# Performance work log

Hardware: AMD Instinct MI355X
Metric: run time of the kernel (lower is better)

Reference implementation:

```python
import jax, jax.numpy as jnp
import numpy as np

N_CODEBOOKS = 4
N_EMBED = 1024
EMBED_DIM = 64
PATCH = 4
BETA = 0.25
EPS = 1e-5
USAGE_W = 0.01


def setup_inputs() -> dict:
    key = jax.random.key(0)
    k1, k2 = jax.random.split(key)
    z = jax.random.normal(k1, (8, 64, 128, 128), dtype=jnp.float32)
    # one EMA codebook per quantizer, initialized ~ randn like torch buffer
    codebooks = jax.random.normal(k2, (N_CODEBOOKS, N_EMBED, EMBED_DIM), dtype=jnp.float32)
    return {"z": z, "codebooks": codebooks}


def _usage_loss(indices, n_embed):
    # negative-entropy penalty on code usage (no gradient path: counts are ints)
    counts = jnp.bincount(indices.reshape(-1), length=n_embed).astype(jnp.float32)
    probs = (counts + EPS) / (counts.sum() + EPS * n_embed)
    entropy = -jnp.sum(probs * jnp.log(probs + EPS))
    return jnp.log(jnp.float32(n_embed)) - entropy


def _ema_quantize(residual, embedding):
    # residual: [N, C, ph, pw], embedding: [n_e, C]; eval mode (no EMA buffer update)
    N, C, ph, pw = residual.shape
    z_flat = residual.transpose(0, 2, 3, 1).reshape(-1, C)  # [M, C]
    d = (jnp.sum(z_flat ** 2, axis=1, keepdims=True)
         + jnp.sum(embedding ** 2, axis=1)
         - 2.0 * z_flat @ embedding.T)  # [M, n_e]
    idx = jnp.argmin(d, axis=1)  # [M]
    z_q = embedding[idx].reshape(N, ph, pw, C).transpose(0, 3, 1, 2)  # [N, C, ph, pw]
    loss = BETA * jnp.mean((jax.lax.stop_gradient(z_q) - residual) ** 2)
    z_q_st = residual + jax.lax.stop_gradient(z_q - residual)  # straight-through
    return z_q_st, loss, idx.reshape(N, ph, pw)


def reference(z, codebooks):
    B, C, H, W = z.shape
    h, w = H // PATCH, W // PATCH
    # b c (h ph) (w pw) -> (b h w) c ph pw
    zp = (z.reshape(B, C, h, PATCH, w, PATCH)
            .transpose(0, 2, 4, 1, 3, 5)
            .reshape(B * h * w, C, PATCH, PATCH))
    zq_acc = jnp.zeros_like(zp)
    residual = zp
    losses, all_idx = [], []
    for i in range(N_CODEBOOKS):
        zq_i, loss_i, idx_i = _ema_quantize(residual, codebooks[i])
        loss_i = loss_i + USAGE_W * _usage_loss(idx_i, N_EMBED)
        zq_acc = zq_acc + zq_i
        residual = residual - zq_i
        losses.append(loss_i)
        all_idx.append(idx_i.reshape(idx_i.shape[0], -1))  # [N, ph*pw]
    loss = jnp.stack(losses).sum()
    # (b h w) c ph pw -> b c (h ph) (w pw)
    z_q = (zq_acc.reshape(B, h, w, C, PATCH, PATCH)
                 .transpose(0, 3, 1, 4, 2, 5)
                 .reshape(B, C, H, W))
    # [N, patch_area, n_codebooks] -> [b, h, w, patch_area, n_codebooks]
    min_idx = jnp.stack(all_idx, axis=-1).reshape(B, h, w, PATCH * PATCH, N_CODEBOOKS)
    return z_q, loss, min_idx
```

## Files before the change

kernel.cpp:

```cpp
#include <hip/hip_runtime.h>
#include <math.h>

typedef __attribute__((ext_vector_type(8))) short short8;
typedef __attribute__((ext_vector_type(4))) float f32x4;

#define NCB 4
#define NE 1024
#define DIM 64
#define HW 16384
#define NPIX 131072
#define NWAVES 4096
#define MSE_DENOM 8388608.0f
#define EPSF 1e-5f
#define CHUNK_BYTES 24576
#define CHUNK_SHORTS 12288
#define NCHUNK 16

__device__ __forceinline__ unsigned short f2bf(float x) {
    unsigned u = __float_as_uint(x);
    u += 0x7fffu + ((u >> 16) & 1u);
    return (unsigned short)(u >> 16);
}
__device__ __forceinline__ float bf2f(unsigned short h) {
    return __uint_as_float(((unsigned)h) << 16);
}

__global__ __launch_bounds__(64) void rvq_norms(const float* __restrict__ cb,
                                                float* __restrict__ nrmh) {
    int code = blockIdx.x * 64 + threadIdx.x;
    const float4* row = reinterpret_cast<const float4*>(cb + (size_t)code * DIM);
    float s0 = 0.f, s1 = 0.f, s2 = 0.f, s3 = 0.f;
#pragma unroll
    for (int k = 0; k < 16; ++k) {
        float4 v = row[k];
        s0 = fmaf(v.x, v.x, s0); s1 = fmaf(v.y, v.y, s1);
        s2 = fmaf(v.z, v.z, s2); s3 = fmaf(v.w, v.w, s3);
    }
    nrmh[code] = -0.5f * ((s0 + s1) + (s2 + s3));
}

__global__ __launch_bounds__(256) void rvq_presplit(const float* __restrict__ cb,
                                                    unsigned short* __restrict__ gB) {
    int blk = blockIdx.x;
    int tid = threadIdx.x;
    int code = tid >> 2, dg = tid & 3;
    int c0 = (blk & 15) << 6;
    int i  = blk >> 4;
    const float4* s4 = reinterpret_cast<const float4*>(
        cb + ((size_t)i * NE + c0 + code) * DIM + dg * 16);
    float v[16];
    {
        float4 q;
        q = s4[0]; v[0]=q.x; v[1]=q.y; v[2]=q.z; v[3]=q.w;
        q = s4[1]; v[4]=q.x; v[5]=q.y; v[6]=q.z; v[7]=q.w;
        q = s4[2]; v[8]=q.x; v[9]=q.y; v[10]=q.z; v[11]=q.w;
        q = s4[3]; v[12]=q.x; v[13]=q.y; v[14]=q.z; v[15]=q.w;
    }
    char* outc = reinterpret_cast<char*>(gB + (size_t)blk * CHUNK_SHORTS);
    int linbase = code * 128 + dg * 32;
    int sw = (code & 7) << 4;
#pragma unroll
    for (int h = 0; h < 2; ++h) {
        short8 p1, p2, p3;
#pragma unroll
        for (int e = 0; e < 8; ++e) {
            float t = v[h * 8 + e];
            unsigned short u1 = f2bf(t); t -= bf2f(u1);
            unsigned short u2 = f2bf(t); t -= bf2f(u2);
            unsigned short u3 = f2bf(t);
            p1[e] = (short)u1; p2[e] = (short)u2; p3[e] = (short)u3;
        }
        int a = (linbase + h * 16) ^ sw;
        *reinterpret_cast<short8*>(outc + a)         = p1;
        *reinterpret_cast<short8*>(outc + 8192 + a)  = p2;
        *reinterpret_cast<short8*>(outc + 16384 + a) = p3;
    }
}

__device__ __forceinline__ void gload16(const void* gsrc, void* ldst) {
    __builtin_amdgcn_global_load_lds(
        (const __attribute__((address_space(1))) unsigned int*)gsrc,
        (__attribute__((address_space(3))) unsigned int*)ldst, 16, 0, 0);
}

__global__ __launch_bounds__(256, 2) void rvq_main(
    const float* __restrict__ z, const unsigned short* __restrict__ gB,
    const float* __restrict__ nrmh, const float* __restrict__ cb,
    float* __restrict__ out_zq, float* __restrict__ out_idx,
    unsigned* __restrict__ hist, float* __restrict__ msePartial)
{
    __shared__ uint4 sB[2][CHUNK_BYTES / 16];
    __shared__ int   sBest[4][32];

    const int tid  = threadIdx.x;
    const int lane = tid & 63;
    const int wid  = tid >> 6;
    const int col  = lane & 15;
    const int g    = lane >> 4;
    const int blockPix = blockIdx.x * 128;
    char* sBase = reinterpret_cast<char*>(sB);
    const int sw = (col & 7) << 4;

#pragma unroll
    for (int k = 0; k < 6; ++k)
        gload16(reinterpret_cast<const char*>(gB) + k * 4096 + tid * 16,
                sBase + k * 4096 + tid * 16);

    size_t zb[2];
#pragma unroll
    for (int m = 0; m < 2; ++m) {
        int pf = blockPix + wid * 32 + m * 16 + col;
        zb[m] = (size_t)(pf >> 14) * 1048576 + (size_t)(pf & 16383);
    }

    float r[2][2][8];
#pragma unroll
    for (int m = 0; m < 2; ++m)
#pragma unroll
        for (int kh = 0; kh < 2; ++kh)
#pragma unroll
            for (int e = 0; e < 8; ++e)
                r[m][kh][e] = z[zb[m] + (size_t)(kh * 32 + g * 8 + e) * HW];

    for (int i = 0; i < NCB; ++i) {
        const char* gBi = reinterpret_cast<const char*>(gB) + (size_t)i * NCHUNK * CHUNK_BYTES;
        const float* nrm_i = nrmh + i * NE;

        short8 A[3][2][2];
#pragma unroll
        for (int m = 0; m < 2; ++m)
#pragma unroll
            for (int kh = 0; kh < 2; ++kh)
#pragma unroll
                for (int e = 0; e < 8; ++e) {
                    float t = r[m][kh][e];
                    unsigned short u1 = f2bf(t); t -= bf2f(u1);
                    unsigned short u2 = f2bf(t); t -= bf2f(u2);
                    unsigned short u3 = f2bf(t);
                    A[0][m][kh][e] = (short)u1;
                    A[1][m][kh][e] = (short)u2;
                    A[2][m][kh][e] = (short)u3;
                }

        float maxv[2][4]; int maxi[2][4];
#pragma unroll
        for (int m = 0; m < 2; ++m)
#pragma unroll
            for (int rr = 0; rr < 4; ++rr) { maxv[m][rr] = -3.4e38f; maxi[m][rr] = 0; }

        for (int c = 0; c < NCHUNK; ++c) {
            __syncthreads();
            if (c < NCHUNK - 1) {
                const char* gc = gBi + (size_t)(c + 1) * CHUNK_BYTES;
                char* sbn = sBase + ((c + 1) & 1) * CHUNK_BYTES;
#pragma unroll
                for (int k = 0; k < 6; ++k)
                    gload16(gc + k * 4096 + tid * 16, sbn + k * 4096 + tid * 16);
            }
            const char* sbc = sBase + (c & 1) * CHUNK_BYTES;

#pragma unroll
            for (int sub = 0; sub < 4; ++sub) {
                const int code = (sub << 4) + col;
                float nh = nrm_i[(c << 6) + code];
                f32x4 acc[2];
#pragma unroll
                for (int rr = 0; rr < 4; ++rr) { acc[0][rr] = nh; acc[1][rr] = nh; }

                __builtin_amdgcn_s_setprio(1);
#pragma unroll
                for (int sb = 0; sb < 3; ++sb) {
                    short8 B0 = *reinterpret_cast<const short8*>(
                        sbc + sb * 8192 + ((((code << 7) + (g << 4))) ^ sw));
                    short8 B1 = *reinterpret_cast<const short8*>(
                        sbc + sb * 8192 + ((((code << 7) + 64 + (g << 4))) ^ sw));
#pragma unroll
                    for (int sa = 0; sa < 3 - sb; ++sa) {
                        acc[0] = __builtin_amdgcn_mfma_f32_16x16x32_bf16(A[sa][0][0], B0, acc[0], 0, 0, 0);
                        acc[1] = __builtin_amdgcn_mfma_f32_16x16x32_bf16(A[sa][1][0], B0, acc[1], 0, 0, 0);
                        acc[0] = __builtin_amdgcn_mfma_f32_16x16x32_bf16(A[sa][0][1], B1, acc[0], 0, 0, 0);
                        acc[1] = __builtin_amdgcn_mfma_f32_16x16x32_bf16(A[sa][1][1], B1, acc[1], 0, 0, 0);
                    }
                }
                __builtin_amdgcn_s_setprio(0);

#pragma unroll
                for (int m = 0; m < 2; ++m)
#pragma unroll
                    for (int rr = 0; rr < 4; ++rr) {
                        float s = acc[m][rr];
                        if (s > maxv[m][rr]) { maxv[m][rr] = s; maxi[m][rr] = (c << 6) + code; }
                    }
            }
        }

        if (i < NCB - 1) {
            const char* gn = reinterpret_cast<const char*>(gB)
                           + (size_t)(i + 1) * NCHUNK * CHUNK_BYTES;
#pragma unroll
            for (int k = 0; k < 6; ++k)
                gload16(gn + k * 4096 + tid * 16, sBase + k * 4096 + tid * 16);
        }

#pragma unroll
        for (int m = 0; m < 2; ++m)
#pragma unroll
            for (int rr = 0; rr < 4; ++rr) {
                float v = maxv[m][rr]; int ix = maxi[m][rr];
#pragma unroll
                for (int off = 1; off < 16; off <<= 1) {
                    float ov = __shfl_xor(v, off, 64);
                    int   oi = __shfl_xor(ix, off, 64);
                    if (ov > v || (ov == v && oi < ix)) { v = ov; ix = oi; }
                }
                maxi[m][rr] = ix;
            }
        if (col == 0) {
#pragma unroll
            for (int m = 0; m < 2; ++m)
#pragma unroll
                for (int rr = 0; rr < 4; ++rr)
                    sBest[wid][m * 16 + g * 4 + rr] = maxi[m][rr];
        }

        const float* cbi = cb + (size_t)i * NE * DIM;
        if (lane < 16) {
#pragma unroll
            for (int m = 0; m < 2; ++m) {
                int pfr = blockPix + wid * 32 + m * 16 + lane;
                int bb = pfr >> 14, yy = (pfr >> 7) & 127, xx = pfr & 127;
                int bi = sBest[wid][m * 16 + lane];
                size_t off = (size_t)bb * 65536 + (size_t)(yy >> 2) * 2048
                           + (size_t)(xx >> 2) * 64
                           + (size_t)(((yy & 3) << 2) + (xx & 3)) * 4 + (size_t)i;
                out_idx[off] = (float)bi;
                atomicAdd(&hist[i * NE + bi], 1u);
            }
        }

#pragma unroll
        for (int m = 0; m < 2; ++m) {
            const int best = sBest[wid][m * 16 + col];
            const float* er = cbi + (size_t)best * DIM;
#pragma unroll
            for (int kh = 0; kh < 2; ++kh) {
                const float4* e4 = reinterpret_cast<const float4*>(er + kh * 32 + g * 8);
                float4 q0 = e4[0], q1 = e4[1];
                r[m][kh][0] -= q0.x; r[m][kh][1] -= q0.y;
                r[m][kh][2] -= q0.z; r[m][kh][3] -= q0.w;
                r[m][kh][4] -= q1.x; r[m][kh][5] -= q1.y;
                r[m][kh][6] -= q1.z; r[m][kh][7] -= q1.w;
            }
        }

        float s = 0.f;
#pragma unroll
        for (int m = 0; m < 2; ++m)
#pragma unroll
            for (int kh = 0; kh < 2; ++kh)
#pragma unroll
                for (int e = 0; e < 8; ++e) s = fmaf(r[m][kh][e], r[m][kh][e], s);
#pragma unroll
        for (int d_ = 32; d_ > 0; d_ >>= 1) s += __shfl_down(s, d_, 64);
        if (lane == 0) msePartial[i * NWAVES + blockIdx.x * 4 + wid] = s;
    }

#pragma unroll
    for (int m = 0; m < 2; ++m)
#pragma unroll
        for (int kh = 0; kh < 2; ++kh)
#pragma unroll
            for (int e = 0; e < 8; ++e) {
                size_t o = zb[m] + (size_t)(kh * 32 + g * 8 + e) * HW;
                out_zq[o] = z[o] - r[m][kh][e];
            }
}

__global__ __launch_bounds__(1024) void rvq_finalize(
    const unsigned* __restrict__ hist, const float* __restrict__ msePartial,
    float* __restrict__ out_loss)
{
    __shared__ float red[1024];
    int t = threadIdx.x;
    float loss = 0.f;
    for (int i = 0; i < NCB; ++i) {
        float cnt = (float)hist[i * NE + t];
        float prob = (cnt + EPSF) / (131072.0f + EPSF * 1024.0f);
        red[t] = -prob * logf(prob + EPSF);
        __syncthreads();
        for (int s = 512; s > 0; s >>= 1) { if (t < s) red[t] += red[t + s]; __syncthreads(); }
        float entropy = red[0];
        __syncthreads();
        float acc = 0.f;
#pragma unroll
        for (int k = 0; k < 4; ++k) acc += msePartial[i * NWAVES + k * 1024 + t];
        red[t] = acc;
        __syncthreads();
        for (int s = 512; s > 0; s >>= 1) { if (t < s) red[t] += red[t + s]; __syncthreads(); }
        float mse_sum = red[0];
        __syncthreads();
        loss += 0.25f * (mse_sum / MSE_DENOM) + 0.01f * (logf(1024.0f) - entropy);
    }
    if (t == 0) out_loss[0] = loss;
}

extern "C" void kernel_launch(void* const* d_in, const int* in_sizes, int n_in,
                              void* d_out, int out_size, void* d_ws, size_t ws_size,
                              hipStream_t stream) {
    const float* z  = (const float*)d_in[0];
    const float* cb = (const float*)d_in[1];

    float* out      = (float*)d_out;
    float* out_zq   = out;
    float* out_loss = out + 8388608;
    float* out_idx  = out + 8388609;

    unsigned* hist        = (unsigned*)d_ws;
    float*    nrmh        = (float*)((char*)d_ws + 16384);
    float*    msePartial  = (float*)((char*)d_ws + 32768);
    unsigned short* gB    = (unsigned short*)((char*)d_ws + 163840);

    hipMemsetAsync(d_ws, 0, 16384, stream);
    rvq_norms<<<64, 64, 0, stream>>>(cb, nrmh);
    rvq_presplit<<<64, 256, 0, stream>>>(cb, gB);
    rvq_main<<<1024, 256, 0, stream>>>(z, gB, nrmh, cb, out_zq, out_idx, hist, msePartial);
    rvq_finalize<<<1, 1024, 0, stream>>>(hist, msePartial, out_loss);
}
```

Before: 382.3 us.

## Switch distance GEMM from 16x16x32 to 32x32x16 bf16 MFMA tiles

```diff
diff --git a/kernel.cpp b/kernel.cpp
--- a/kernel.cpp
+++ b/kernel.cpp
@@ -2,7 +2,7 @@
 #include <math.h>
 
 typedef __attribute__((ext_vector_type(8))) short short8;
-typedef __attribute__((ext_vector_type(4))) float f32x4;
+typedef __attribute__((ext_vector_type(16))) float f32x16;
 
 #define NCB 4
 #define NE 1024
@@ -95,58 +95,48 @@
     const int tid  = threadIdx.x;
     const int lane = tid & 63;
     const int wid  = tid >> 6;
-    const int col  = lane & 15;
-    const int g    = lane >> 4;
+    const int q    = lane & 31;
+    const int h    = lane >> 5;
     const int blockPix = blockIdx.x * 128;
     char* sBase = reinterpret_cast<char*>(sB);
-    const int sw = (col & 7) << 4;
+    const int sw = (q & 7) << 4;
 
 #pragma unroll
     for (int k = 0; k < 6; ++k)
         gload16(reinterpret_cast<const char*>(gB) + k * 4096 + tid * 16,
                 sBase + k * 4096 + tid * 16);
 
-    size_t zb[2];
-#pragma unroll
-    for (int m = 0; m < 2; ++m) {
-        int pf = blockPix + wid * 32 + m * 16 + col;
-        zb[m] = (size_t)(pf >> 14) * 1048576 + (size_t)(pf & 16383);
-    }
-
-    float r[2][2][8];
-#pragma unroll
-    for (int m = 0; m < 2; ++m)
-#pragma unroll
-        for (int kh = 0; kh < 2; ++kh)
-#pragma unroll
-            for (int e = 0; e < 8; ++e)
-                r[m][kh][e] = z[zb[m] + (size_t)(kh * 32 + g * 8 + e) * HW];
+    const int pf = blockPix + wid * 32 + q;
+    const size_t zb = (size_t)(pf >> 14) * 1048576 + (size_t)(pf & 16383);
+
+    float r[4][8];
+#pragma unroll
+    for (int kb = 0; kb < 4; ++kb)
+#pragma unroll
+        for (int e = 0; e < 8; ++e)
+            r[kb][e] = z[zb + (size_t)(kb * 16 + h * 8 + e) * HW];
 
     for (int i = 0; i < NCB; ++i) {
         const char* gBi = reinterpret_cast<const char*>(gB) + (size_t)i * NCHUNK * CHUNK_BYTES;
         const float* nrm_i = nrmh + i * NE;
 
-        short8 A[3][2][2];
-#pragma unroll
-        for (int m = 0; m < 2; ++m)
-#pragma unroll
-            for (int kh = 0; kh < 2; ++kh)
-#pragma unroll
-                for (int e = 0; e < 8; ++e) {
-                    float t = r[m][kh][e];
-                    unsigned short u1 = f2bf(t); t -= bf2f(u1);
-                    unsigned short u2 = f2bf(t); t -= bf2f(u2);
-                    unsigned short u3 = f2bf(t);
-                    A[0][m][kh][e] = (short)u1;
-                    A[1][m][kh][e] = (short)u2;
-                    A[2][m][kh][e] = (short)u3;
-                }
-
-        float maxv[2][4]; int maxi[2][4];
-#pragma unroll
-        for (int m = 0; m < 2; ++m)
-#pragma unroll
-            for (int rr = 0; rr < 4; ++rr) { maxv[m][rr] = -3.4e38f; maxi[m][rr] = 0; }
+        short8 A[3][4];
+#pragma unroll
+        for (int kb = 0; kb < 4; ++kb)
+#pragma unroll
+            for (int e = 0; e < 8; ++e) {
+                float t = r[kb][e];
+                unsigned short u1 = f2bf(t); t -= bf2f(u1);
+                unsigned short u2 = f2bf(t); t -= bf2f(u2);
+                unsigned short u3 = f2bf(t);
+                A[0][kb][e] = (short)u1;
+                A[1][kb][e] = (short)u2;
+                A[2][kb][e] = (short)u3;
+            }
+
+        float maxv[16]; int maxi[16];
+#pragma unroll
+        for (int rr = 0; rr < 16; ++rr) { maxv[rr] = -3.4e38f; maxi[rr] = 0; }
 
         for (int c = 0; c < NCHUNK; ++c) {
             __syncthreads();
@@ -160,37 +150,34 @@
             const char* sbc = sBase + (c & 1) * CHUNK_BYTES;
 
 #pragma unroll
-            for (int sub = 0; sub < 4; ++sub) {
-                const int code = (sub << 4) + col;
-                float nh = nrm_i[(c << 6) + code];
-                f32x4 acc[2];
-#pragma unroll
-                for (int rr = 0; rr < 4; ++rr) { acc[0][rr] = nh; acc[1][rr] = nh; }
+            for (int b = 0; b < 2; ++b) {
+                const int code = (c << 6) + (b << 5) + q;
+                float nh = nrm_i[code];
+                f32x16 acc;
+#pragma unroll
+                for (int rr = 0; rr < 16; ++rr) acc[rr] = nh;
 
                 __builtin_amdgcn_s_setprio(1);
 #pragma unroll
                 for (int sb = 0; sb < 3; ++sb) {
-                    short8 B0 = *reinterpret_cast<const short8*>(
-                        sbc + sb * 8192 + ((((code << 7) + (g << 4))) ^ sw));
-                    short8 B1 = *reinterpret_cast<const short8*>(
-                        sbc + sb * 8192 + ((((code << 7) + 64 + (g << 4))) ^ sw));
-#pragma unroll
-                    for (int sa = 0; sa < 3 - sb; ++sa) {
-                        acc[0] = __builtin_amdgcn_mfma_f32_16x16x32_bf16(A[sa][0][0], B0, acc[0], 0, 0, 0);
-                        acc[1] = __builtin_amdgcn_mfma_f32_16x16x32_bf16(A[sa][1][0], B0, acc[1], 0, 0, 0);
-                        acc[0] = __builtin_amdgcn_mfma_f32_16x16x32_bf16(A[sa][0][1], B1, acc[0], 0, 0, 0);
-                        acc[1] = __builtin_amdgcn_mfma_f32_16x16x32_bf16(A[sa][1][1], B1, acc[1], 0, 0, 0);
+#pragma unroll
+                    for (int kb = 0; kb < 4; ++kb) {
+                        short8 Bf = *reinterpret_cast<const short8*>(
+                            sbc + sb * 8192 +
+                            (((b << 12) + (q << 7) + kb * 32 + h * 16) ^ sw));
+#pragma unroll
+                        for (int sa = 0; sa < 3 - sb; ++sa)
+                            acc = __builtin_amdgcn_mfma_f32_32x32x16_bf16(
+                                A[sa][kb], Bf, acc, 0, 0, 0);
                     }
                 }
                 __builtin_amdgcn_s_setprio(0);
 
 #pragma unroll
-                for (int m = 0; m < 2; ++m)
-#pragma unroll
-                    for (int rr = 0; rr < 4; ++rr) {
-                        float s = acc[m][rr];
-                        if (s > maxv[m][rr]) { maxv[m][rr] = s; maxi[m][rr] = (c << 6) + code; }
-                    }
+                for (int rr = 0; rr < 16; ++rr) {
+                    float s = acc[rr];
+                    if (s > maxv[rr]) { maxv[rr] = s; maxi[rr] = code; }
+                }
             }
         }
 
@@ -203,77 +190,67 @@
         }
 
 #pragma unroll
-        for (int m = 0; m < 2; ++m)
-#pragma unroll
-            for (int rr = 0; rr < 4; ++rr) {
-                float v = maxv[m][rr]; int ix = maxi[m][rr];
-#pragma unroll
-                for (int off = 1; off < 16; off <<= 1) {
-                    float ov = __shfl_xor(v, off, 64);
-                    int   oi = __shfl_xor(ix, off, 64);
-                    if (ov > v || (ov == v && oi < ix)) { v = ov; ix = oi; }
-                }
-                maxi[m][rr] = ix;
-            }
-        if (col == 0) {
-#pragma unroll
-            for (int m = 0; m < 2; ++m)
-#pragma unroll
-                for (int rr = 0; rr < 4; ++rr)
-                    sBest[wid][m * 16 + g * 4 + rr] = maxi[m][rr];
+        for (int rr = 0; rr < 16; ++rr) {
+            float v = maxv[rr]; int ix = maxi[rr];
+#pragma unroll
+            for (int off = 1; off < 32; off <<= 1) {
+                float ov = __shfl_xor(v, off, 64);
+                int   oi = __shfl_xor(ix, off, 64);
+                if (ov > v || (ov == v && oi < ix)) { v = ov; ix = oi; }
+            }
+            maxi[rr] = ix;
+        }
+        if (q == 0) {
+#pragma unroll
+            for (int rr = 0; rr < 16; ++rr) {
+                int row = (rr & 3) + 8 * (rr >> 2) + 4 * h;
+                sBest[wid][row] = maxi[rr];
+            }
         }
 
         const float* cbi = cb + (size_t)i * NE * DIM;
-        if (lane < 16) {
-#pragma unroll
-            for (int m = 0; m < 2; ++m) {
-                int pfr = blockPix + wid * 32 + m * 16 + lane;
-                int bb = pfr >> 14, yy = (pfr >> 7) & 127, xx = pfr & 127;
-                int bi = sBest[wid][m * 16 + lane];
-                size_t off = (size_t)bb * 65536 + (size_t)(yy >> 2) * 2048
-                           + (size_t)(xx >> 2) * 64
-                           + (size_t)(((yy & 3) << 2) + (xx & 3)) * 4 + (size_t)i;
-                out_idx[off] = (float)bi;
-                atomicAdd(&hist[i * NE + bi], 1u);
-            }
-        }
-
-#pragma unroll
-        for (int m = 0; m < 2; ++m) {
-            const int best = sBest[wid][m * 16 + col];
-            const float* er = cbi + (size_t)best * DIM;
-#pragma unroll
-            for (int kh = 0; kh < 2; ++kh) {
-                const float4* e4 = reinterpret_cast<const float4*>(er + kh * 32 + g * 8);
-                float4 q0 = e4[0], q1 = e4[1];
-                r[m][kh][0] -= q0.x; r[m][kh][1] -= q0.y;
-                r[m][kh][2] -= q0.z; r[m][kh][3] -= q0.w;
-                r[m][kh][4] -= q1.x; r[m][kh][5] -= q1.y;
-                r[m][kh][6] -= q1.z; r[m][kh][7] -= q1.w;
+        if (lane < 32) {
+            int pfr = blockPix + wid * 32 + lane;
+            int bb = pfr >> 14, yy = (pfr >> 7) & 127, xx = pfr & 127;
+            int bi = sBest[wid][lane];
+            size_t off = (size_t)bb * 65536 + (size_t)(yy >> 2) * 2048
+                       + (size_t)(xx >> 2) * 64
+                       + (size_t)(((yy & 3) << 2) + (xx & 3)) * 4 + (size_t)i;
+            out_idx[off] = (float)bi;
+            atomicAdd(&hist[i * NE + bi], 1u);
+        }
+
+        {
+            const int best = sBest[wid][q];
+            const float* er = cbi + (size_t)best * DIM + h * 8;
+#pragma unroll
+            for (int kb = 0; kb < 4; ++kb) {
+                float4 q0 = *reinterpret_cast<const float4*>(er + kb * 16);
+                float4 q1 = *reinterpret_cast<const float4*>(er + kb * 16 + 4);
+                r[kb][0] -= q0.x; r[kb][1] -= q0.y;
+                r[kb][2] -= q0.z; r[kb][3] -= q0.w;
+                r[kb][4] -= q1.x; r[kb][5] -= q1.y;
+                r[kb][6] -= q1.z; r[kb][7] -= q1.w;
             }
         }
 
         float s = 0.f;
 #pragma unroll
-        for (int m = 0; m < 2; ++m)
-#pragma unroll
-            for (int kh = 0; kh < 2; ++kh)
-#pragma unroll
-                for (int e = 0; e < 8; ++e) s = fmaf(r[m][kh][e], r[m][kh][e], s);
+        for (int kb = 0; kb < 4; ++kb)
+#pragma unroll
+            for (int e = 0; e < 8; ++e) s = fmaf(r[kb][e], r[kb][e], s);
 #pragma unroll
         for (int d_ = 32; d_ > 0; d_ >>= 1) s += __shfl_down(s, d_, 64);
         if (lane == 0) msePartial[i * NWAVES + blockIdx.x * 4 + wid] = s;
     }
 
 #pragma unroll
-    for (int m = 0; m < 2; ++m)
-#pragma unroll
-        for (int kh = 0; kh < 2; ++kh)
-#pragma unroll
-            for (int e = 0; e < 8; ++e) {
-                size_t o = zb[m] + (size_t)(kh * 32 + g * 8 + e) * HW;
-                out_zq[o] = z[o] - r[m][kh][e];
-            }
+    for (int kb = 0; kb < 4; ++kb)
+#pragma unroll
+        for (int e = 0; e < 8; ++e) {
+            size_t o = zb + (size_t)(kb * 16 + h * 8 + e) * HW;
+            out_zq[o] = z[o] - r[kb][e];
+        }
 }
 
 __global__ __launch_bounds__(1024) void rvq_finalize(
```

Result: slower. 424.9 us (+11.2%).
